# Kernel tuning notes

Measured on AMD Instinct MI355X. Metric: run time of the kernel, lower is better.

## Reference

```python
import jax, jax.numpy as jnp
import numpy as np

P_DROP = 0.2
N_NODES, N_EDGES, FEAT, HID, NUM_CLASSES = 100000, 1600000, 128, 128, 40


def setup_inputs() -> dict:
    key = jax.random.key(0)
    k1, k2, k3, k4 = jax.random.split(key, 4)
    x = jax.random.normal(k1, (N_NODES, FEAT), dtype=jnp.float32)
    edge_index = jax.random.randint(k2, (2, N_EDGES), 0, N_NODES, dtype=jnp.int32)
    W1 = jax.random.normal(k3, (FEAT, HID), dtype=jnp.float32) / np.sqrt(FEAT).astype(np.float32)
    b1 = jnp.zeros((HID,), jnp.float32)
    W2 = jax.random.normal(k4, (HID, NUM_CLASSES), dtype=jnp.float32) / np.sqrt(HID).astype(np.float32)
    b2 = jnp.zeros((NUM_CLASSES,), jnp.float32)
    return {"x": x, "edge_index": edge_index, "W1": W1, "b1": b1, "W2": W2, "b2": b2}


def _dropout(x, key, p):
    # F.dropout with training=True (the torch functional default used in the module)
    keep = jax.random.bernoulli(key, 1.0 - p, x.shape)
    return jnp.where(keep, x / (1.0 - p), jnp.zeros((), x.dtype))


def _gcn_conv(x, W, b, src, dst, n):
    # PyG GCNConv: add self-loops, symmetric normalization D^-1/2 A D^-1/2, then W x + b
    h = x @ W                                                   # [N, out]
    deg = jax.ops.segment_sum(jnp.ones_like(dst, dtype=h.dtype), dst, num_segments=n) + 1.0
    dinv = jax.lax.rsqrt(deg)                                   # [N]
    norm = dinv[src] * dinv[dst]                                # [E]
    agg = jax.ops.segment_sum(h[src] * norm[:, None], dst, num_segments=n)
    agg = agg + h * (dinv * dinv)[:, None]                      # self-loop term
    return agg + b


def reference(x, edge_index, W1, b1, W2, b2):
    src, dst = edge_index[0], edge_index[1]
    n = x.shape[0]
    kd1, kd2 = jax.random.split(jax.random.key(42))
    h = jax.nn.relu(_dropout(x, kd1, P_DROP))
    h = _gcn_conv(h, W1, b1, src, dst, n)
    h = jax.nn.relu(_dropout(h, kd2, P_DROP))
    h = _gcn_conv(h, W2, b2, src, dst, n)
    return h
```

## Files before the change

kernel.cpp:

```cpp
#include <hip/hip_runtime.h>
#include <stdint.h>

__host__ __device__ inline void tf2x32(unsigned k0, unsigned k1,
                                       unsigned& x0, unsigned& x1) {
  unsigned k2 = k0 ^ k1 ^ 0x1BD11BDAu;
  x0 += k0; x1 += k1;
#define TFR(r) { x0 += x1; x1 = (x1 << (r)) | (x1 >> (32 - (r))); x1 ^= x0; }
  TFR(13) TFR(15) TFR(26) TFR(6)
  x0 += k1; x1 += k2 + 1u;
  TFR(17) TFR(29) TFR(16) TFR(24)
  x0 += k2; x1 += k0 + 2u;
  TFR(13) TFR(15) TFR(26) TFR(6)
  x0 += k0; x1 += k1 + 3u;
  TFR(17) TFR(29) TFR(16) TFR(24)
  x0 += k1; x1 += k2 + 4u;
  TFR(13) TFR(15) TFR(26) TFR(6)
  x0 += k2; x1 += k0 + 5u;
#undef TFR
}

__device__ __forceinline__ float drop_scale(unsigned k0, unsigned k1, unsigned f) {
  unsigned a = 0u, b = f;
  tf2x32(k0, k1, a, b);
  unsigned bits = a ^ b;
  float u = __uint_as_float((bits >> 9) | 0x3f800000u) - 1.0f;
  return (u < 0.8f) ? 1.25f : 0.0f;
}

__device__ __forceinline__ unsigned f2bf(float x) {
  unsigned u = __float_as_uint(x);
  return (u + 0x7fffu + ((u >> 16) & 1u)) >> 16;
}
__device__ __forceinline__ float bf_lo(unsigned u) { return __uint_as_float(u << 16); }
__device__ __forceinline__ float bf_hi(unsigned u) { return __uint_as_float(u & 0xffff0000u); }

__global__ __launch_bounds__(256) void count_rank(
    const int* __restrict__ dst, int* __restrict__ cnt,
    int* __restrict__ rank, int e) {
  int i0 = (blockIdx.x * 256 + threadIdx.x) * 4;
  if (i0 + 3 < e) {
    int4 d4 = *(const int4*)&dst[i0];
    int4 r4;
    r4.x = atomicAdd(&cnt[d4.x], 1);
    r4.y = atomicAdd(&cnt[d4.y], 1);
    r4.z = atomicAdd(&cnt[d4.z], 1);
    r4.w = atomicAdd(&cnt[d4.w], 1);
    *(int4*)&rank[i0] = r4;
  } else {
    for (int i = i0; i < e; ++i)
      rank[i] = atomicAdd(&cnt[dst[i]], 1);
  }
}

__global__ __launch_bounds__(256) void fill_adj_cursor(
    const int* __restrict__ src, const int* __restrict__ dst,
    int* __restrict__ cursor, int* __restrict__ adj, int e) {
  int i0 = (blockIdx.x * 256 + threadIdx.x) * 4;
  for (int i = i0; i < min(i0 + 4, e); ++i) {
    int d = dst[i];
    int p = atomicAdd(&cursor[d], 1);
    adj[p] = src[i];
  }
}

__global__ void scan_local(const int* __restrict__ cnt, int* __restrict__ excl,
                           int* __restrict__ bsum, float* __restrict__ dinv, int n) {
  __shared__ int sh[512];
  int i = blockIdx.x * 512 + threadIdx.x;
  int v = (i < n) ? cnt[i] : 0;
  if (i < n) dinv[i] = 1.0f / sqrtf((float)v + 1.0f);
  sh[threadIdx.x] = v;
  __syncthreads();
  for (int d = 1; d < 512; d <<= 1) {
    int t = (threadIdx.x >= d) ? sh[threadIdx.x - d] : 0;
    __syncthreads();
    sh[threadIdx.x] += t;
    __syncthreads();
  }
  if (i < n) excl[i] = sh[threadIdx.x] - v;
  if (threadIdx.x == 511) bsum[blockIdx.x] = sh[511];
}

__global__ void scan_bsum(int* __restrict__ bsum, int nb) {
  __shared__ int sh[256];
  int tid = threadIdx.x;
  int v = (tid < nb) ? bsum[tid] : 0;
  sh[tid] = v;
  __syncthreads();
  for (int d = 1; d < 256; d <<= 1) {
    int t = (tid >= d) ? sh[tid - d] : 0;
    __syncthreads();
    sh[tid] += t;
    __syncthreads();
  }
  if (tid < nb) bsum[tid] = sh[tid] - v;
}

__global__ void scan_final(const int* __restrict__ excl, const int* __restrict__ bsum,
                           int* __restrict__ rowptr, int* __restrict__ cursor,
                           int n, int e, int write_cursor) {
  int i = blockIdx.x * blockDim.x + threadIdx.x;
  if (i < n) {
    int r = excl[i] + bsum[i >> 9];
    rowptr[i] = r;
    if (write_cursor) cursor[i] = r;
  }
  if (i == n) rowptr[n] = e;
}

__global__ __launch_bounds__(256) void fill_csr(
    const int* __restrict__ src, const int* __restrict__ dst,
    const int* __restrict__ rank, const int* __restrict__ rowptr,
    int* __restrict__ adj, int e) {
  int i0 = (blockIdx.x * 256 + threadIdx.x) * 8;
  if (i0 + 7 < e) {
    int4 d0 = *(const int4*)&dst[i0];
    int4 d1 = *(const int4*)&dst[i0 + 4];
    int4 r0 = *(const int4*)&rank[i0];
    int4 r1 = *(const int4*)&rank[i0 + 4];
    int4 s0 = *(const int4*)&src[i0];
    int4 s1 = *(const int4*)&src[i0 + 4];
    int p0 = rowptr[d0.x] + r0.x;
    int p1 = rowptr[d0.y] + r0.y;
    int p2 = rowptr[d0.z] + r0.z;
    int p3 = rowptr[d0.w] + r0.w;
    int p4 = rowptr[d1.x] + r1.x;
    int p5 = rowptr[d1.y] + r1.y;
    int p6 = rowptr[d1.z] + r1.z;
    int p7 = rowptr[d1.w] + r1.w;
    adj[p0] = s0.x; adj[p1] = s0.y; adj[p2] = s0.z; adj[p3] = s0.w;
    adj[p4] = s1.x; adj[p5] = s1.y; adj[p6] = s1.z; adj[p7] = s1.w;
  } else {
    for (int i = i0; i < e; ++i)
      adj[rowptr[dst[i]] + rank[i]] = src[i];
  }
}

__global__ __launch_bounds__(256) void gemm_l1(
    const float* __restrict__ A, const float* __restrict__ W,
    const float* __restrict__ dinv, unsigned short* __restrict__ Hout,
    int n, unsigned kd0, unsigned kd1)
{
  __shared__ float Ash[32 * 128];
  __shared__ float Wsh[32 * 128];
  const int tid = threadIdx.x;
  const int r0 = blockIdx.x * 32;
  const float4* W4 = (const float4*)W;
  float4* Ws4 = (float4*)Wsh;

  for (int i4 = tid; i4 < 32 * 32; i4 += 256) {
    int rr = i4 >> 5;
    int k4 = (i4 & 31) << 2;
    int row = r0 + rr;
    float4 v = make_float4(0.f, 0.f, 0.f, 0.f);
    if (row < n) {
      v = *(const float4*)&A[(size_t)row * 128 + k4];
      unsigned fb = (unsigned)row * 128u + (unsigned)k4;
      float* pv = &v.x;
#pragma unroll
      for (int j = 0; j < 4; ++j)
        pv[j] = fmaxf(pv[j], 0.0f) * drop_scale(kd0, kd1, fb + j);
    }
    *(float4*)&Ash[rr * 128 + k4] = v;
  }
  for (int i = tid; i < 1024; i += 256) Ws4[i] = W4[i];
  __syncthreads();

  const int tx = tid & 31, ty = tid >> 5;
  const int c0 = tx * 4;
  const int rl = ty * 4;
  float acc[4][4] = {};
  for (int kb = 0; kb < 4; ++kb) {
    if (kb) {
      __syncthreads();
      for (int i = tid; i < 1024; i += 256) Ws4[i] = W4[kb * 1024 + i];
      __syncthreads();
    }
    const int kbase = kb * 32;
    for (int k = 0; k < 32; k += 4) {
      float4 a[4];
#pragma unroll
      for (int i = 0; i < 4; ++i)
        a[i] = *(const float4*)&Ash[(rl + i) * 128 + kbase + k];
#pragma unroll
      for (int kk = 0; kk < 4; ++kk) {
        float4 w = *(const float4*)&Wsh[(k + kk) * 128 + c0];
#pragma unroll
        for (int i = 0; i < 4; ++i) {
          float av = (&a[i].x)[kk];
          acc[i][0] += av * w.x; acc[i][1] += av * w.y;
          acc[i][2] += av * w.z; acc[i][3] += av * w.w;
        }
      }
    }
  }

#pragma unroll
  for (int i = 0; i < 4; ++i) {
    int row = r0 + rl + i;
    if (row < n) {
      float di = dinv[row];
      uint2 p;
      p.x = f2bf(acc[i][0] * di) | (f2bf(acc[i][1] * di) << 16);
      p.y = f2bf(acc[i][2] * di) | (f2bf(acc[i][3] * di) << 16);
      *(uint2*)&Hout[(size_t)row * 128 + c0] = p;
    }
  }
}

template<bool FUSE_F>
__global__ __launch_bounds__(256) void pull128k(
    const unsigned short* __restrict__ H, const int* __restrict__ rowptr,
    const int* __restrict__ adj, const float* __restrict__ dinv,
    const float* __restrict__ bias, unsigned short* __restrict__ Out,
    int n, unsigned k0, unsigned k1)
{
  int wid = (blockIdx.x * 256 + threadIdx.x) >> 6;
  int lane = threadIdx.x & 63;
  if (wid >= n) return;
  int beg = rowptr[wid], end = rowptr[wid + 1];
  const unsigned* Hu = (const unsigned*)H;
  unsigned su = Hu[(size_t)wid * 64 + lane];
  float2 acc[8];
  acc[0] = make_float2(bf_lo(su), bf_hi(su));
#pragma unroll
  for (int k = 1; k < 8; ++k) acc[k] = make_float2(0.f, 0.f);

  int last = end - 1;
  for (int j = beg; j < end; j += 8) {
    int idx[8];
#pragma unroll
    for (int k = 0; k < 8; ++k) idx[k] = adj[min(j + k, last)];
    unsigned u[8];
#pragma unroll
    for (int k = 0; k < 8; ++k)
      u[k] = Hu[(size_t)idx[k] * 64 + lane];
#pragma unroll
    for (int k = 0; k < 8; ++k) {
      if (j + k <= last) { acc[k].x += bf_lo(u[k]); acc[k].y += bf_hi(u[k]); }
    }
  }

  float sx = ((acc[0].x + acc[1].x) + (acc[2].x + acc[3].x)) +
             ((acc[4].x + acc[5].x) + (acc[6].x + acc[7].x));
  float sy = ((acc[0].y + acc[1].y) + (acc[2].y + acc[3].y)) +
             ((acc[4].y + acc[5].y) + (acc[6].y + acc[7].y));
  float di = dinv[wid];
  unsigned c = (unsigned)lane * 2u;
  float o0, o1;
  if (FUSE_F) {
    float s1a = sx * di + bias[c];
    float s1b = sy * di + bias[c + 1];
    unsigned fb = (unsigned)wid * 128u + c;
    o0 = di * fmaxf(s1a * drop_scale(k0, k1, fb), 0.0f);
    o1 = di * fmaxf(s1b * drop_scale(k0, k1, fb + 1u), 0.0f);
  } else {
    o0 = sx * di;
    o1 = sy * di;
  }
  ((unsigned*)Out)[(size_t)wid * 64 + lane] = f2bf(o0) | (f2bf(o1) << 16);
}

__global__ __launch_bounds__(256) void gemm_out(
    const unsigned short* __restrict__ G, const float* __restrict__ W2,
    const float* __restrict__ b2, float* __restrict__ out, int n)
{
  __shared__ float Ash[64 * 128];
  __shared__ float Wsh[32 * 64];
  const int tid = threadIdx.x;
  const int r0 = blockIdx.x * 64;
  const uint2* G2 = (const uint2*)G;

  for (int i = tid; i < 64 * 32; i += 256) {
    int rr = i >> 5, q = i & 31;
    int row = r0 + rr;
    uint2 g = make_uint2(0u, 0u);
    if (row < n) g = G2[(size_t)row * 32 + q];
    float* d = &Ash[rr * 128 + q * 4];
    d[0] = bf_lo(g.x); d[1] = bf_hi(g.x);
    d[2] = bf_lo(g.y); d[3] = bf_hi(g.y);
  }

  const int tx = tid & 15, ty = tid >> 4;
  const int c0 = tx * 4;
  const int rl = ty * 4;
  float acc[4][4] = {};
  for (int kb = 0; kb < 4; ++kb) {
    __syncthreads();
    for (int i = tid; i < 2048; i += 256) {
      int r = i >> 6, c = i & 63;
      Wsh[i] = (c < 40) ? W2[(kb * 32 + r) * 40 + c] : 0.0f;
    }
    __syncthreads();
    const int kbase = kb * 32;
    for (int k = 0; k < 32; k += 4) {
      float4 a[4];
#pragma unroll
      for (int i = 0; i < 4; ++i)
        a[i] = *(const float4*)&Ash[(rl + i) * 128 + kbase + k];
#pragma unroll
      for (int kk = 0; kk < 4; ++kk) {
        float4 w = *(const float4*)&Wsh[(k + kk) * 64 + c0];
#pragma unroll
        for (int i = 0; i < 4; ++i) {
          float av = (&a[i].x)[kk];
          acc[i][0] += av * w.x; acc[i][1] += av * w.y;
          acc[i][2] += av * w.z; acc[i][3] += av * w.w;
        }
      }
    }
  }

  if (c0 < 40) {
#pragma unroll
    for (int i = 0; i < 4; ++i) {
      int row = r0 + rl + i;
      if (row < n) {
        float4 o = make_float4(acc[i][0] + b2[c0],     acc[i][1] + b2[c0 + 1],
                               acc[i][2] + b2[c0 + 2], acc[i][3] + b2[c0 + 3]);
        *(float4*)&out[(size_t)row * 40 + c0] = o;
      }
    }
  }
}

extern "C" void kernel_launch(void* const* d_in, const int* in_sizes, int n_in,
                              void* d_out, int out_size, void* d_ws, size_t ws_size,
                              hipStream_t stream) {
  const float* x  = (const float*)d_in[0];
  const int*   ei = (const int*)d_in[1];
  const float* W1 = (const float*)d_in[2];
  const float* b1 = (const float*)d_in[3];
  const float* W2 = (const float*)d_in[4];
  const float* b2 = (const float*)d_in[5];
  const int n = in_sizes[0] / 128;
  const int e = in_sizes[1] / 2;
  const int* src = ei;
  const int* dst = ei + e;

  unsigned kd1a = 0u, kd1b = 0u; tf2x32(0u, 42u, kd1a, kd1b);
  unsigned kd2a = 0u, kd2b = 1u; tf2x32(0u, 42u, kd2a, kd2b);

  char* wsp = (char*)d_ws;
  size_t off = 0;
  auto take = [&](size_t bytes) -> char* {
    char* p = wsp + off;
    off = (off + bytes + 255) & ~(size_t)255;
    return p;
  };
  int*   cnt    = (int*)take((size_t)n * 4);
  int*   excl   = (int*)take((size_t)n * 4);
  int*   bsum   = (int*)take(1024);
  int*   rowptr = (int*)take((size_t)(n + 1) * 4);
  float* dinv   = (float*)take((size_t)n * 4);
  int*   adj    = (int*)take((size_t)e * 4);
  unsigned short* Hb = (unsigned short*)take((size_t)n * 128 * 2);
  unsigned short* Fb = (unsigned short*)take((size_t)n * 128 * 2);
  size_t base_off = off;
  int*   rank   = (int*)take((size_t)e * 4);
  bool use_rank = (off <= ws_size);
  int*   cursor = use_rank ? nullptr : (int*)(wsp + base_off);
  (void)n_in; (void)out_size;

  hipMemsetAsync(cnt, 0, (size_t)n * 4, stream);
  if (use_rank) {
    count_rank<<<(e / 4 + 256) / 256, 256, 0, stream>>>(dst, cnt, rank, e);
  } else {
    count_rank<<<(e / 4 + 256) / 256, 256, 0, stream>>>(dst, cnt, cursor, e);
  }
  int nblk = (n + 511) / 512;
  scan_local<<<nblk, 512, 0, stream>>>(cnt, excl, bsum, dinv, n);
  scan_bsum<<<1, 256, 0, stream>>>(bsum, nblk);
  scan_final<<<(n + 256) / 256, 256, 0, stream>>>(excl, bsum, rowptr, cursor,
                                                  n, e, use_rank ? 0 : 1);
  if (use_rank) {
    fill_csr<<<(e / 8 + 256) / 256, 256, 0, stream>>>(src, dst, rank, rowptr, adj, e);
  } else {
    fill_adj_cursor<<<(e / 4 + 256) / 256, 256, 0, stream>>>(src, dst, cursor, adj, e);
  }

  gemm_l1<<<(n + 31) / 32, 256, 0, stream>>>(x, W1, dinv, Hb, n, kd1a, kd1b);

  pull128k<true><<<(n + 3) / 4, 256, 0, stream>>>(Hb, rowptr, adj, dinv, b1,
                                                  Fb, n, kd2a, kd2b);

  pull128k<false><<<(n + 3) / 4, 256, 0, stream>>>(Fb, rowptr, adj, dinv, b1,
                                                   Hb, n, 0u, 0u);

  gemm_out<<<(n + 63) / 64, 256, 0, stream>>>(Hb, W2, b2, (float*)d_out, n);
}
```

Baseline: 458.3 us.

## Use bf16 MFMA for layer-1 GEMM with swizzled LDS tiles

Replaces the fp32 scalar-FMA layer-1 GEMM with a bf16 MFMA 16x16x32 kernel. A small new kernel first transposes W1 into bf16. The GEMM stages the dropout-applied inputs and W1 in XOR-swizzled LDS and writes the output back through LDS for coalesced stores. This cuts the FMA cost of the dense GEMM and doubles rows per block. In exchange the GEMM inputs are rounded to bf16 before multiplying, which loses precision, and it adds one extra kernel launch.

```diff
diff --git a/kernel.cpp b/kernel.cpp
--- a/kernel.cpp
+++ b/kernel.cpp
@@ -1,5 +1,8 @@
 #include <hip/hip_runtime.h>
 #include <stdint.h>
+
+typedef __attribute__((ext_vector_type(8))) short bf16x8;
+typedef __attribute__((ext_vector_type(4))) float f32x4;
 
 __host__ __device__ inline void tf2x32(unsigned k0, unsigned k1,
                                        unsigned& x0, unsigned& x1) {
@@ -136,74 +139,113 @@
   }
 }
 
-__global__ __launch_bounds__(256) void gemm_l1(
-    const float* __restrict__ A, const float* __restrict__ W,
+__global__ __launch_bounds__(256) void w1t_bf16(
+    const float* __restrict__ W, unsigned short* __restrict__ Wt) {
+  int i = blockIdx.x * 256 + threadIdx.x;
+  int k = i >> 7, c = i & 127;
+  Wt[c * 128 + k] = (unsigned short)f2bf(W[i]);
+}
+
+__global__ __launch_bounds__(256) void gemm_l1_mfma(
+    const float* __restrict__ A, const unsigned short* __restrict__ Wt,
     const float* __restrict__ dinv, unsigned short* __restrict__ Hout,
     int n, unsigned kd0, unsigned kd1)
 {
-  __shared__ float Ash[32 * 128];
-  __shared__ float Wsh[32 * 128];
+  __shared__ unsigned short Ash[64 * 128];
+  __shared__ unsigned short Wsh[128 * 128];
   const int tid = threadIdx.x;
-  const int r0 = blockIdx.x * 32;
-  const float4* W4 = (const float4*)W;
-  float4* Ws4 = (float4*)Wsh;
-
-  for (int i4 = tid; i4 < 32 * 32; i4 += 256) {
-    int rr = i4 >> 5;
-    int k4 = (i4 & 31) << 2;
-    int row = r0 + rr;
-    float4 v = make_float4(0.f, 0.f, 0.f, 0.f);
-    if (row < n) {
-      v = *(const float4*)&A[(size_t)row * 128 + k4];
-      unsigned fb = (unsigned)row * 128u + (unsigned)k4;
-      float* pv = &v.x;
-#pragma unroll
-      for (int j = 0; j < 4; ++j)
-        pv[j] = fmaxf(pv[j], 0.0f) * drop_scale(kd0, kd1, fb + j);
-    }
-    *(float4*)&Ash[rr * 128 + k4] = v;
-  }
-  for (int i = tid; i < 1024; i += 256) Ws4[i] = W4[i];
+  const int r0 = blockIdx.x * 64;
+
+  {
+    const uint4* Wg = (const uint4*)Wt;
+    uint4* Ws = (uint4*)Wsh;
+    for (int j = tid; j < 2048; j += 256) {
+      int row = j >> 4, ch = j & 15;
+      Ws[row * 16 + (ch ^ (row & 7))] = Wg[j];
+    }
+  }
+
+  {
+    uint4* As = (uint4*)Ash;
+    for (int j = tid; j < 1024; j += 256) {
+      int row = j >> 4, ch = j & 15;
+      int grow = r0 + row;
+      uint4 pk = make_uint4(0u, 0u, 0u, 0u);
+      if (grow < n) {
+        const float4* p = (const float4*)&A[(size_t)grow * 128 + ch * 8];
+        float4 f0 = p[0], f1 = p[1];
+        unsigned fb = (unsigned)grow * 128u + (unsigned)(ch * 8);
+        float a0 = fmaxf(f0.x, 0.f) * drop_scale(kd0, kd1, fb + 0u);
+        float a1 = fmaxf(f0.y, 0.f) * drop_scale(kd0, kd1, fb + 1u);
+        float a2 = fmaxf(f0.z, 0.f) * drop_scale(kd0, kd1, fb + 2u);
+        float a3 = fmaxf(f0.w, 0.f) * drop_scale(kd0, kd1, fb + 3u);
+        float a4 = fmaxf(f1.x, 0.f) * drop_scale(kd0, kd1, fb + 4u);
+        float a5 = fmaxf(f1.y, 0.f) * drop_scale(kd0, kd1, fb + 5u);
+        float a6 = fmaxf(f1.z, 0.f) * drop_scale(kd0, kd1, fb + 6u);
+        float a7 = fmaxf(f1.w, 0.f) * drop_scale(kd0, kd1, fb + 7u);
+        pk.x = f2bf(a0) | (f2bf(a1) << 16);
+        pk.y = f2bf(a2) | (f2bf(a3) << 16);
+        pk.z = f2bf(a4) | (f2bf(a5) << 16);
+        pk.w = f2bf(a6) | (f2bf(a7) << 16);
+      }
+      As[row * 16 + (ch ^ (row & 7))] = pk;
+    }
+  }
   __syncthreads();
 
-  const int tx = tid & 31, ty = tid >> 5;
-  const int c0 = tx * 4;
-  const int rl = ty * 4;
-  float acc[4][4] = {};
-  for (int kb = 0; kb < 4; ++kb) {
-    if (kb) {
-      __syncthreads();
-      for (int i = tid; i < 1024; i += 256) Ws4[i] = W4[kb * 1024 + i];
-      __syncthreads();
-    }
-    const int kbase = kb * 32;
-    for (int k = 0; k < 32; k += 4) {
-      float4 a[4];
-#pragma unroll
-      for (int i = 0; i < 4; ++i)
-        a[i] = *(const float4*)&Ash[(rl + i) * 128 + kbase + k];
-#pragma unroll
-      for (int kk = 0; kk < 4; ++kk) {
-        float4 w = *(const float4*)&Wsh[(k + kk) * 128 + c0];
-#pragma unroll
-        for (int i = 0; i < 4; ++i) {
-          float av = (&a[i].x)[kk];
-          acc[i][0] += av * w.x; acc[i][1] += av * w.y;
-          acc[i][2] += av * w.z; acc[i][3] += av * w.w;
-        }
-      }
-    }
-  }
-
-#pragma unroll
-  for (int i = 0; i < 4; ++i) {
-    int row = r0 + rl + i;
-    if (row < n) {
-      float di = dinv[row];
-      uint2 p;
-      p.x = f2bf(acc[i][0] * di) | (f2bf(acc[i][1] * di) << 16);
-      p.y = f2bf(acc[i][2] * di) | (f2bf(acc[i][3] * di) << 16);
-      *(uint2*)&Hout[(size_t)row * 128 + c0] = p;
+  const int w = tid >> 6, l = tid & 63;
+  const int hk = l >> 4;
+  const int rl = w * 16 + (l & 15);
+  const bf16x8* A8 = (const bf16x8*)Ash;
+  const bf16x8* W8 = (const bf16x8*)Wsh;
+
+  bf16x8 afr[4];
+#pragma unroll
+  for (int ks = 0; ks < 4; ++ks)
+    afr[ks] = A8[rl * 16 + ((ks * 4 + hk) ^ (rl & 7))];
+
+  f32x4 acc[8];
+#pragma unroll
+  for (int nf = 0; nf < 8; ++nf) acc[nf] = (f32x4){0.f, 0.f, 0.f, 0.f};
+
+#pragma unroll
+  for (int nf = 0; nf < 8; ++nf) {
+    int col = nf * 16 + (l & 15);
+    int cb = col * 16, cs = col & 7;
+#pragma unroll
+    for (int ks = 0; ks < 4; ++ks) {
+      bf16x8 b = W8[cb + ((ks * 4 + hk) ^ cs)];
+      acc[nf] = __builtin_amdgcn_mfma_f32_16x16x32_bf16(afr[ks], b, acc[nf], 0, 0, 0);
+    }
+  }
+
+  float di[4];
+  const int rbase = r0 + w * 16 + hk * 4;
+#pragma unroll
+  for (int r = 0; r < 4; ++r) {
+    int gr = rbase + r;
+    di[r] = (gr < n) ? dinv[gr] : 0.f;
+  }
+#pragma unroll
+  for (int nf = 0; nf < 8; ++nf) {
+    int colb = nf * 16 + (l & 15);
+#pragma unroll
+    for (int r = 0; r < 4; ++r) {
+      int lrow = w * 16 + hk * 4 + r;
+      unsigned byteoff = (unsigned)(lrow * 256 + colb * 2);
+      byteoff ^= (unsigned)((lrow & 7) << 4);
+      *(unsigned short*)((char*)Ash + byteoff) =
+          (unsigned short)f2bf(acc[nf][r] * di[r]);
+    }
+  }
+  __syncthreads();
+
+  for (int j = tid; j < 1024; j += 256) {
+    int row = j >> 4, ch = j & 15;
+    int grow = r0 + row;
+    if (grow < n) {
+      uint4 v = ((const uint4*)Ash)[row * 16 + (ch ^ (row & 7))];
+      *(uint4*)&Hout[(size_t)grow * 128 + ch * 8] = v;
     }
   }
 }
@@ -356,6 +398,7 @@
   int*   adj    = (int*)take((size_t)e * 4);
   unsigned short* Hb = (unsigned short*)take((size_t)n * 128 * 2);
   unsigned short* Fb = (unsigned short*)take((size_t)n * 128 * 2);
+  unsigned short* Wt = (unsigned short*)take(128 * 128 * 2);
   size_t base_off = off;
   int*   rank   = (int*)take((size_t)e * 4);
   bool use_rank = (off <= ws_size);
@@ -379,7 +422,9 @@
     fill_adj_cursor<<<(e / 4 + 256) / 256, 256, 0, stream>>>(src, dst, cursor, adj, e);
   }
 
-  gemm_l1<<<(n + 31) / 32, 256, 0, stream>>>(x, W1, dinv, Hb, n, kd1a, kd1b);
+  w1t_bf16<<<64, 256, 0, stream>>>(W1, Wt);
+
+  gemm_l1_mfma<<<(n + 63) / 64, 256, 0, stream>>>(x, Wt, dinv, Hb, n, kd1a, kd1b);
 
   pull128k<true><<<(n + 3) / 4, 256, 0, stream>>>(Hb, rowptr, adj, dinv, b1,
                                                   Fb, n, kd2a, kd2b);
```

After: 438.1 us. 4.4% less time.
